# Kernel optimization log

Measured on AMD Instinct MI355X. Metric: run time of the kernel, lower is better.

The kernel has to match this reference:

```python
import jax, jax.numpy as jnp
import numpy as np
import math

L, H, P = 16384, 128, 256


def setup_inputs() -> dict:
    key = jax.random.key(0)
    k = jax.random.split(key, 6)
    return {
        "input_sequence": jax.random.normal(k[0], (L, H), dtype=jnp.float32),
        "A_diag": jax.random.uniform(k[1], (P,), dtype=jnp.float32),
        "B": (jax.random.uniform(k[2], (P, H, 2), dtype=jnp.float32) * 2.0 - 1.0) / math.sqrt(H),
        "C": (jax.random.uniform(k[3], (H, P, 2), dtype=jnp.float32) * 2.0 - 1.0) / math.sqrt(P),
        "D": jax.random.normal(k[4], (H,), dtype=jnp.float32),
        "steps": jax.random.uniform(k[5], (P,), dtype=jnp.float32),
    }


def _binop(qi, qj):
    # 2x2 block-diagonal matrix product + affine state propagation, per channel.
    iA, iB, iC, iD, ib1, ib2 = qi
    jA, jB, jC, jD, jb1, jb2 = qj
    return (
        jA * iA + jB * iC,
        jA * iB + jB * iD,
        jC * iA + jD * iC,
        jC * iB + jD * iD,
        jA * ib1 + jB * ib2 + jb1,
        jC * ib1 + jD * ib2 + jb2,
    )


def reference(input_sequence, A_diag, B, C, D, steps):
    # LinOSS-IM discretization (implicit)
    A = jax.nn.relu(A_diag)                      # (P,)
    dt = jax.nn.sigmoid(steps)                   # (P,)
    Bc = B[..., 0] + 1j * B[..., 1]              # (P,H) complex64
    Cc = C[..., 0] + 1j * C[..., 1]              # (H,P) complex64

    Bu = input_sequence @ Bc.T                   # (L,P) complex64

    schur = 1.0 / (1.0 + dt ** 2 * A)
    M11 = 1.0 - dt ** 2 * A * schur
    M12 = -dt * A * schur
    M21 = dt * schur
    M22 = schur

    ones = jnp.ones((input_sequence.shape[0], A.shape[0]), dtype=input_sequence.dtype)
    F1 = M11 * Bu * dt                           # (L,P) complex
    F2 = M21 * Bu * dt

    elems = (M11 * ones, M12 * ones, M21 * ones, M22 * ones, F1, F2)
    _, _, _, _, _, x2 = jax.lax.associative_scan(_binop, elems)  # scan over L

    ys = jnp.real(x2 @ Cc.T)                     # (L,H)
    return ys + input_sequence * D
```

## Files before the change

### kernel.cpp

```cpp
#include <hip/hip_runtime.h>
#include <math.h>

#define L 16384
#define H 128
#define P 256
#define CL 32
#define NCH (L/CL)
#define GS 16
#define NG (NCH/GS)
#define KDIM 512
#define NBU 512

typedef __attribute__((ext_vector_type(8))) short short8;
typedef __attribute__((ext_vector_type(4))) float f32x4;

__device__ inline unsigned short f2bf(float f){
  union { float f; unsigned u; } v; v.f = f;
  unsigned u = v.u;
  u += 0x7fffu + ((u >> 16) & 1u);
  return (unsigned short)(u >> 16);
}
__device__ inline float bf2f(unsigned short s){
  union { unsigned u; float f; } v; v.u = ((unsigned)s) << 16;
  return v.f;
}

struct Params { float M11,M12,M21,M22,s1,s2; };

__device__ inline Params get_params(const float* A_diag, const float* steps, int p){
  float A = A_diag[p]; A = A > 0.f ? A : 0.f;
  float dt = 1.f/(1.f + expf(-steps[p]));
  float schur = 1.f/(1.f + dt*dt*A);
  Params q;
  q.M11 = 1.f - dt*dt*A*schur;
  q.M12 = -dt*A*schur;
  q.M21 = dt*schur;
  q.M22 = schur;
  q.s1 = q.M11*dt;
  q.s2 = q.M21*dt;
  return q;
}

__device__ inline unsigned long long aload(const unsigned long long* p){
  return __hip_atomic_load((unsigned long long*)p, __ATOMIC_RELAXED,
                           __HIP_MEMORY_SCOPE_AGENT);
}
__device__ inline void apub(unsigned long long* p, unsigned long long v){
  (void)__hip_atomic_exchange(p, v, __ATOMIC_RELAXED, __HIP_MEMORY_SCOPE_AGENT);
}
__device__ inline void fpub(unsigned* p){
  (void)__hip_atomic_exchange(p, 1u, __ATOMIC_RELAXED, __HIP_MEMORY_SCOPE_AGENT);
}
__device__ inline void wait_flag(unsigned* f){
  while (__hip_atomic_load(f, __ATOMIC_RELAXED, __HIP_MEMORY_SCOPE_AGENT) == 0u)
    __builtin_amdgcn_s_sleep(2);
}

__global__ __launch_bounds__(512) void prep_w(const float* __restrict__ B,
                                              const float* __restrict__ Cw,
                                              unsigned short* __restrict__ BWswz,
                                              unsigned short* __restrict__ Bswz,
                                              unsigned* __restrict__ flags){
  int gidx = blockIdx.x*512 + threadIdx.x;
  if (gidx < NCH + NG) flags[gidx] = 0u;
  if (gidx < H*NBU){
    int k = gidx >> 9, n = gidx & 511;
    int p = n & 255, c2 = n >> 8;
    float v = B[((size_t)p*H + k)*2 + c2];
    BWswz[((size_t)(k>>3)*NBU + n)*8 + (k&7)] = f2bf(v);
  } else {
    int g2 = gidx - H*NBU;
    int k = g2 >> 7, n = g2 & 127;
    float v = (k < P) ? Cw[((size_t)n*P + k)*2]
                      : -Cw[((size_t)n*P + (k-P))*2 + 1];
    Bswz[((size_t)(k>>3)*H + n)*8 + (k&7)] = f2bf(v);
  }
}

__global__ __launch_bounds__(512, 4) void linoss_fused(
    const float* __restrict__ in,
    const float* __restrict__ A_diag,
    const float* __restrict__ steps,
    const float* __restrict__ Dv,
    const unsigned short* __restrict__ BWswz,
    const unsigned short* __restrict__ Bswz,
    unsigned long long* __restrict__ finals,
    unsigned long long* __restrict__ gfin,
    unsigned* __restrict__ flag1,
    unsigned* __restrict__ flag2,
    float* __restrict__ out)
{
  __shared__ unsigned short sX[CL][NBU+8];
  const int c   = blockIdx.x;
  const int tid = threadIdx.x;

  {
    int lane = tid & 63, w = tid >> 6;
    int ml = lane & 15, quad = lane >> 4;
    int mt = w & 1, ng = w >> 1;
    int lm0 = mt*16;
    const float* aptr = in + (size_t)(c*CL + lm0 + ml)*H + quad*8;
    short8 av[4];
    #pragma unroll
    for (int ks=0; ks<4; ks++){
      float4 f0 = *(const float4*)(aptr + ks*32);
      float4 f1 = *(const float4*)(aptr + ks*32 + 4);
      union { short8 s; unsigned short u[8]; } o;
      o.u[0]=f2bf(f0.x); o.u[1]=f2bf(f0.y); o.u[2]=f2bf(f0.z); o.u[3]=f2bf(f0.w);
      o.u[4]=f2bf(f1.x); o.u[5]=f2bf(f1.y); o.u[6]=f2bf(f1.z); o.u[7]=f2bf(f1.w);
      av[ks] = o.s;
    }
    f32x4 acc[8];
    #pragma unroll
    for (int t=0;t<8;t++) acc[t] = (f32x4){0.f,0.f,0.f,0.f};
    #pragma unroll
    for (int ks=0; ks<4; ks++){
      #pragma unroll
      for (int t=0;t<8;t++){
        int n0 = (ng*8 + t)*16;
        short8 bv = *(const short8*)(BWswz + ((size_t)(ks*4+quad)*NBU + n0 + ml)*8);
        acc[t] = __builtin_amdgcn_mfma_f32_16x16x32_bf16(av[ks], bv, acc[t], 0, 0, 0);
      }
    }
    #pragma unroll
    for (int t=0;t<8;t++){
      int n = (ng*8+t)*16 + ml;
      #pragma unroll
      for (int r=0;r<4;r++)
        sX[lm0 + quad*4 + r][n] = f2bf(acc[t][r]);
    }
  }
  __syncthreads();

  const int p = tid & 255, part = tid >> 8;
  Params q = get_params(A_diag, steps, p);
  float Ta=q.M11, Tb=q.M12, Tc=q.M21, Td=q.M22;
  #pragma unroll
  for (int s=0;s<5;s++){
    float na=Ta*Ta+Tb*Tc, nb=Ta*Tb+Tb*Td, nc=Tc*Ta+Td*Tc, nd=Tc*Tb+Td*Td;
    Ta=na;Tb=nb;Tc=nc;Td=nd;
  }
  float fx1=0.f, fx2=0.f;
  {
    #pragma unroll
    for (int i=0;i<CL;i++){
      float u = bf2f(sX[i][part*256 + p]);
      float n1 = q.M11*fx1 + q.M12*fx2 + q.s1*u;
      float n2 = q.M21*fx1 + q.M22*fx2 + q.s2*u;
      fx1 = n1; fx2 = n2;
    }
    union { unsigned long long u; float2 f; } w; w.f = make_float2(fx1,fx2);
    apub(&finals[(size_t)(part*NCH + c)*P + p], w.u);
  }
  asm volatile("s_waitcnt vmcnt(0)" ::: "memory");
  __syncthreads();
  if (tid == 0) fpub(&flag1[c]);

  const int g = c >> 4, iw = c & (GS-1);
  const unsigned long long* Fp = finals + (size_t)part*NCH*P + (size_t)g*GS*P + p;

  float z1=0.f, z2v=0.f;
  bool have_z = false;
  if (iw == GS-1){
    if (tid < GS-1) wait_flag(&flag1[g*GS + tid]);
    __syncthreads();
    unsigned long long v[GS-1];
    #pragma unroll
    for (int j=0;j<GS-1;j++) v[j] = aload(Fp + (size_t)j*P);
    #pragma unroll
    for (int j=0;j<GS-1;j++){
      union { unsigned long long u; float2 f; } w; w.u = v[j];
      float n1 = Ta*z1 + Tb*z2v + w.f.x;
      float n2 = Tc*z1 + Td*z2v + w.f.y;
      z1=n1; z2v=n2;
    }
    have_z = true;
    float t1 = Ta*z1 + Tb*z2v + fx1;
    float t2 = Tc*z1 + Td*z2v + fx2;
    union { unsigned long long u; float2 f; } w; w.f = make_float2(t1,t2);
    apub(&gfin[(size_t)(part*NG + g)*P + p], w.u);
    asm volatile("s_waitcnt vmcnt(0)" ::: "memory");
    __syncthreads();
    if (tid == 0) fpub(&flag2[g]);
  }

  float sa=1.f, sb=0.f, sc=0.f, sd=1.f;
  {
    float wa=Ta, wb=Tb, wc=Tc, wd=Td;
    #pragma unroll
    for (int bit=0; bit<4; bit++){
      if ((iw>>bit)&1){
        float na = wa*sa + wb*sc, nb = wa*sb + wb*sd;
        float nc = wc*sa + wd*sc, nd = wc*sb + wd*sd;
        sa=na; sb=nb; sc=nc; sd=nd;
      }
      float qa = wa*wa + wb*wc, qb = wa*wb + wb*wd;
      float qc = wc*wa + wd*wc, qd = wc*wb + wd*wd;
      wa=qa; wb=qb; wc=qc; wd=qd;
    }
  }
  float ga=Ta, gb=Tb, gc=Tc, gd=Td;
  #pragma unroll
  for (int s=0;s<4;s++){
    float na=ga*ga+gb*gc, nb=ga*gb+gb*gd, nc=gc*ga+gd*gc, nd=gc*gb+gd*gd;
    ga=na;gb=nb;gc=nc;gd=nd;
  }

  if (tid < g)                             wait_flag(&flag2[tid]);
  if (!have_z && tid >= 64 && tid < 64+iw) wait_flag(&flag1[g*GS + (tid-64)]);
  __syncthreads();

  {
    float y1=0.f, y2=0.f;
    {
      const unsigned long long* Gp = gfin + (size_t)part*NG*P + p;
      for (int t0=0; t0<g; t0+=8){
        unsigned long long v[8];
        #pragma unroll
        for (int j=0;j<8;j++){
          int jj = t0+j;
          v[j] = (jj < g) ? aload(Gp + (size_t)jj*P) : 0ULL;
        }
        #pragma unroll
        for (int j=0;j<8;j++){
          int jj = t0+j;
          if (jj < g){
            union { unsigned long long u; float2 f; } w; w.u = v[j];
            float n1 = ga*y1 + gb*y2 + w.f.x;
            float n2 = gc*y1 + gd*y2 + w.f.y;
            y1=n1; y2=n2;
          }
        }
      }
    }
    if (!have_z){
      for (int t0=0; t0<iw; t0+=8){
        unsigned long long v[8];
        #pragma unroll
        for (int j=0;j<8;j++){
          int jj = t0+j;
          v[j] = (jj < iw) ? aload(Fp + (size_t)jj*P) : 0ULL;
        }
        #pragma unroll
        for (int j=0;j<8;j++){
          int jj = t0+j;
          if (jj < iw){
            union { unsigned long long u; float2 f; } w; w.u = v[j];
            float n1 = Ta*z1 + Tb*z2v + w.f.x;
            float n2 = Tc*z1 + Td*z2v + w.f.y;
            z1=n1; z2v=n2;
          }
        }
      }
    }
    float x1 = sa*y1 + sb*y2 + z1;
    float x2 = sc*y1 + sd*y2 + z2v;
    #pragma unroll
    for (int i=0;i<CL;i++){
      float u = bf2f(sX[i][part*256 + p]);
      float n1 = q.M11*x1 + q.M12*x2 + q.s1*u;
      float n2 = q.M21*x1 + q.M22*x2 + q.s2*u;
      x1 = n1; x2 = n2;
      sX[i][part*256 + p] = f2bf(x2);
    }
  }
  __syncthreads();

  {
    int lane = tid & 63, w = tid >> 6;
    int ml = lane & 15, quad = lane >> 4;
    int mt = w & 1;
    int ntb = (w >> 1) * 2;
    f32x4 acc[2];
    acc[0] = (f32x4){0.f,0.f,0.f,0.f};
    acc[1] = (f32x4){0.f,0.f,0.f,0.f};
    for (int ks=0; ks<KDIM/32; ks++){
      short8 av = *(const short8*)&sX[mt*16 + ml][ks*32 + quad*8];
      #pragma unroll
      for (int j=0;j<2;j++){
        short8 bv = *(const short8*)(Bswz + ((size_t)(ks*4+quad)*H + (ntb+j)*16 + ml)*8);
        acc[j] = __builtin_amdgcn_mfma_f32_16x16x32_bf16(av, bv, acc[j], 0, 0, 0);
      }
    }
    #pragma unroll
    for (int j=0;j<2;j++){
      int h = (ntb+j)*16 + ml;
      float dv = Dv[h];
      #pragma unroll
      for (int r=0;r<4;r++){
        int l = c*CL + mt*16 + quad*4 + r;
        out[(size_t)l*H + h] = acc[j][r] + in[(size_t)l*H + h]*dv;
      }
    }
  }
}

extern "C" void kernel_launch(void* const* d_in, const int* in_sizes, int n_in,
                              void* d_out, int out_size, void* d_ws, size_t ws_size,
                              hipStream_t stream) {
  const float* in     = (const float*)d_in[0];
  const float* A_diag = (const float*)d_in[1];
  const float* B      = (const float*)d_in[2];
  const float* Cw     = (const float*)d_in[3];
  const float* Dv     = (const float*)d_in[4];
  const float* steps  = (const float*)d_in[5];
  float* out = (float*)d_out;

  unsigned short* BWswz = (unsigned short*)d_ws;
  unsigned short* Bswz  = BWswz + (size_t)H*NBU;
  unsigned long long* finals = (unsigned long long*)(Bswz + (size_t)KDIM*H);
  unsigned long long* gfin   = finals + (size_t)2*NCH*P;
  unsigned* flags = (unsigned*)(gfin + (size_t)2*NG*P);
  unsigned* flag1 = flags;
  unsigned* flag2 = flags + NCH;

  prep_w<<<256, 512, 0, stream>>>(B, Cw, BWswz, Bswz, flags);
  linoss_fused<<<NCH, 512, 0, stream>>>(in, A_diag, steps, Dv, BWswz, Bswz,
                                        finals, gfin, flag1, flag2, out);
}
```

Before: 100.5 us.

## Double chunk length to 64 and fully unroll cross-chunk carry loads

Doubles the per-block chunk length, which halves the number of chunks and groups. That shrinks the inter-block carry chain and the flag synchronization traffic. The warp-to-tile mappings of both MFMA phases are remapped to cover 64 rows, and the power-of-transition exponent is bumped to match. Carry loads from group and chunk finals are now issued all at once into register arrays rather than in batches of 8. The costs are higher register and LDS pressure (occupancy hint lowered from 4 to 2), longer serial in-block scans, and fewer blocks to fill the GPU.

```diff
diff --git a/kernel.cpp b/kernel.cpp
--- a/kernel.cpp
+++ b/kernel.cpp
@@ -4,7 +4,7 @@
 #define L 16384
 #define H 128
 #define P 256
-#define CL 32
+#define CL 64
 #define NCH (L/CL)
 #define GS 16
 #define NG (NCH/GS)
@@ -53,7 +53,7 @@
 }
 __device__ inline void wait_flag(unsigned* f){
   while (__hip_atomic_load(f, __ATOMIC_RELAXED, __HIP_MEMORY_SCOPE_AGENT) == 0u)
-    __builtin_amdgcn_s_sleep(2);
+    __builtin_amdgcn_s_sleep(1);
 }
 
 __global__ __launch_bounds__(512) void prep_w(const float* __restrict__ B,
@@ -77,7 +77,7 @@
   }
 }
 
-__global__ __launch_bounds__(512, 4) void linoss_fused(
+__global__ __launch_bounds__(512, 2) void linoss_fused(
     const float* __restrict__ in,
     const float* __restrict__ A_diag,
     const float* __restrict__ steps,
@@ -97,8 +97,8 @@
   {
     int lane = tid & 63, w = tid >> 6;
     int ml = lane & 15, quad = lane >> 4;
-    int mt = w & 1, ng = w >> 1;
-    int lm0 = mt*16;
+    int rt = w & 3, ch = w >> 2;
+    int lm0 = rt*16;
     const float* aptr = in + (size_t)(c*CL + lm0 + ml)*H + quad*8;
     short8 av[4];
     #pragma unroll
@@ -110,21 +110,21 @@
       o.u[4]=f2bf(f1.x); o.u[5]=f2bf(f1.y); o.u[6]=f2bf(f1.z); o.u[7]=f2bf(f1.w);
       av[ks] = o.s;
     }
-    f32x4 acc[8];
-    #pragma unroll
-    for (int t=0;t<8;t++) acc[t] = (f32x4){0.f,0.f,0.f,0.f};
+    f32x4 acc[16];
+    #pragma unroll
+    for (int t=0;t<16;t++) acc[t] = (f32x4){0.f,0.f,0.f,0.f};
     #pragma unroll
     for (int ks=0; ks<4; ks++){
       #pragma unroll
-      for (int t=0;t<8;t++){
-        int n0 = (ng*8 + t)*16;
+      for (int t=0;t<16;t++){
+        int n0 = ch*256 + t*16;
         short8 bv = *(const short8*)(BWswz + ((size_t)(ks*4+quad)*NBU + n0 + ml)*8);
         acc[t] = __builtin_amdgcn_mfma_f32_16x16x32_bf16(av[ks], bv, acc[t], 0, 0, 0);
       }
     }
     #pragma unroll
-    for (int t=0;t<8;t++){
-      int n = (ng*8+t)*16 + ml;
+    for (int t=0;t<16;t++){
+      int n = ch*256 + t*16 + ml;
       #pragma unroll
       for (int r=0;r<4;r++)
         sX[lm0 + quad*4 + r][n] = f2bf(acc[t][r]);
@@ -136,7 +136,7 @@
   Params q = get_params(A_diag, steps, p);
   float Ta=q.M11, Tb=q.M12, Tc=q.M21, Td=q.M22;
   #pragma unroll
-  for (int s=0;s<5;s++){
+  for (int s=0;s<6;s++){
     float na=Ta*Ta+Tb*Tc, nb=Ta*Tb+Tb*Td, nc=Tc*Ta+Td*Tc, nd=Tc*Tb+Td*Td;
     Ta=na;Tb=nb;Tc=nc;Td=nd;
   }
@@ -211,45 +211,32 @@
   __syncthreads();
 
   {
+    const unsigned long long* Gp = gfin + (size_t)part*NG*P + p;
+    unsigned long long vy[NG-1], vm[GS-1];
+    #pragma unroll
+    for (int j=0;j<NG-1;j++) vy[j] = (j < g) ? aload(Gp + (size_t)j*P) : 0ULL;
+    if (!have_z){
+      #pragma unroll
+      for (int j=0;j<GS-1;j++) vm[j] = (j < iw) ? aload(Fp + (size_t)j*P) : 0ULL;
+    }
     float y1=0.f, y2=0.f;
-    {
-      const unsigned long long* Gp = gfin + (size_t)part*NG*P + p;
-      for (int t0=0; t0<g; t0+=8){
-        unsigned long long v[8];
-        #pragma unroll
-        for (int j=0;j<8;j++){
-          int jj = t0+j;
-          v[j] = (jj < g) ? aload(Gp + (size_t)jj*P) : 0ULL;
-        }
-        #pragma unroll
-        for (int j=0;j<8;j++){
-          int jj = t0+j;
-          if (jj < g){
-            union { unsigned long long u; float2 f; } w; w.u = v[j];
-            float n1 = ga*y1 + gb*y2 + w.f.x;
-            float n2 = gc*y1 + gd*y2 + w.f.y;
-            y1=n1; y2=n2;
-          }
-        }
+    #pragma unroll
+    for (int j=0;j<NG-1;j++){
+      if (j < g){
+        union { unsigned long long u; float2 f; } w; w.u = vy[j];
+        float n1 = ga*y1 + gb*y2 + w.f.x;
+        float n2 = gc*y1 + gd*y2 + w.f.y;
+        y1=n1; y2=n2;
       }
     }
     if (!have_z){
-      for (int t0=0; t0<iw; t0+=8){
-        unsigned long long v[8];
-        #pragma unroll
-        for (int j=0;j<8;j++){
-          int jj = t0+j;
-          v[j] = (jj < iw) ? aload(Fp + (size_t)jj*P) : 0ULL;
-        }
-        #pragma unroll
-        for (int j=0;j<8;j++){
-          int jj = t0+j;
-          if (jj < iw){
-            union { unsigned long long u; float2 f; } w; w.u = v[j];
-            float n1 = Ta*z1 + Tb*z2v + w.f.x;
-            float n2 = Tc*z1 + Td*z2v + w.f.y;
-            z1=n1; z2v=n2;
-          }
+      #pragma unroll
+      for (int j=0;j<GS-1;j++){
+        if (j < iw){
+          union { unsigned long long u; float2 f; } w; w.u = vm[j];
+          float n1 = Ta*z1 + Tb*z2v + w.f.x;
+          float n2 = Tc*z1 + Td*z2v + w.f.y;
+          z1=n1; z2v=n2;
         }
       }
     }
@@ -269,26 +256,26 @@
   {
     int lane = tid & 63, w = tid >> 6;
     int ml = lane & 15, quad = lane >> 4;
-    int mt = w & 1;
-    int ntb = (w >> 1) * 2;
-    f32x4 acc[2];
-    acc[0] = (f32x4){0.f,0.f,0.f,0.f};
-    acc[1] = (f32x4){0.f,0.f,0.f,0.f};
+    int rt2 = w & 3;
+    int nh  = w >> 2;
+    f32x4 acc[4];
+    #pragma unroll
+    for (int j=0;j<4;j++) acc[j] = (f32x4){0.f,0.f,0.f,0.f};
     for (int ks=0; ks<KDIM/32; ks++){
-      short8 av = *(const short8*)&sX[mt*16 + ml][ks*32 + quad*8];
-      #pragma unroll
-      for (int j=0;j<2;j++){
-        short8 bv = *(const short8*)(Bswz + ((size_t)(ks*4+quad)*H + (ntb+j)*16 + ml)*8);
+      short8 av = *(const short8*)&sX[rt2*16 + ml][ks*32 + quad*8];
+      #pragma unroll
+      for (int j=0;j<4;j++){
+        short8 bv = *(const short8*)(Bswz + ((size_t)(ks*4+quad)*H + (nh*4+j)*16 + ml)*8);
         acc[j] = __builtin_amdgcn_mfma_f32_16x16x32_bf16(av, bv, acc[j], 0, 0, 0);
       }
     }
     #pragma unroll
-    for (int j=0;j<2;j++){
-      int h = (ntb+j)*16 + ml;
+    for (int j=0;j<4;j++){
+      int h = (nh*4+j)*16 + ml;
       float dv = Dv[h];
       #pragma unroll
       for (int r=0;r<4;r++){
-        int l = c*CL + mt*16 + quad*4 + r;
+        int l = c*CL + rt2*16 + quad*4 + r;
         out[(size_t)l*H + h] = acc[j][r] + in[(size_t)l*H + h]*dv;
       }
     }
```

Result: faster. 94.36 us (-6.1%).

## Assign chunk IDs by atomic ticket and batch LDS reads in scan loops

Applied to the files above, without the earlier changes.

Each block now takes its chunk index from a global atomic counter instead of blockIdx, so the decoupled look-back cannot wait on chunks whose blocks have not been scheduled yet. The scan loops first read all CL inputs from LDS into registers and write results back in a batch. The group-prefix and in-group loops are fully unrolled with fixed-size loads, and the spin-wait sleep is shortened. This raises register pressure, costs one extra atomic per block, and issues some unneeded loads.

```diff
diff --git a/kernel.cpp b/kernel.cpp
--- a/kernel.cpp
+++ b/kernel.cpp
@@ -53,7 +53,47 @@
 }
 __device__ inline void wait_flag(unsigned* f){
   while (__hip_atomic_load(f, __ATOMIC_RELAXED, __HIP_MEMORY_SCOPE_AGENT) == 0u)
-    __builtin_amdgcn_s_sleep(2);
+    __builtin_amdgcn_s_sleep(1);
+}
+
+__device__ inline void chunk_bu_to_lds(int c, const float* __restrict__ in,
+                                       const unsigned short* __restrict__ BWswz,
+                                       unsigned short (*sBu)[NBU+8]){
+  int tid = threadIdx.x;
+  int lane = tid & 63, w = tid >> 6;
+  int ml = lane & 15, quad = lane >> 4;
+  int mt = w & 1, ng = w >> 1;
+  int lm0 = mt*16;
+  const float* aptr = in + (size_t)(c*CL + lm0 + ml)*H + quad*8;
+  short8 av[4];
+  #pragma unroll
+  for (int ks=0; ks<4; ks++){
+    float4 f0 = *(const float4*)(aptr + ks*32);
+    float4 f1 = *(const float4*)(aptr + ks*32 + 4);
+    union { short8 s; unsigned short u[8]; } o;
+    o.u[0]=f2bf(f0.x); o.u[1]=f2bf(f0.y); o.u[2]=f2bf(f0.z); o.u[3]=f2bf(f0.w);
+    o.u[4]=f2bf(f1.x); o.u[5]=f2bf(f1.y); o.u[6]=f2bf(f1.z); o.u[7]=f2bf(f1.w);
+    av[ks] = o.s;
+  }
+  f32x4 acc[8];
+  #pragma unroll
+  for (int t=0;t<8;t++) acc[t] = (f32x4){0.f,0.f,0.f,0.f};
+  #pragma unroll
+  for (int ks=0; ks<4; ks++){
+    #pragma unroll
+    for (int t=0;t<8;t++){
+      int n0 = (ng*8 + t)*16;
+      short8 bv = *(const short8*)(BWswz + ((size_t)(ks*4+quad)*NBU + n0 + ml)*8);
+      acc[t] = __builtin_amdgcn_mfma_f32_16x16x32_bf16(av[ks], bv, acc[t], 0, 0, 0);
+    }
+  }
+  #pragma unroll
+  for (int t=0;t<8;t++){
+    int n = (ng*8+t)*16 + ml;
+    #pragma unroll
+    for (int r=0;r<4;r++)
+      sBu[lm0 + quad*4 + r][n] = f2bf(acc[t][r]);
+  }
 }
 
 __global__ __launch_bounds__(512) void prep_w(const float* __restrict__ B,
@@ -62,7 +102,7 @@
                                               unsigned short* __restrict__ Bswz,
                                               unsigned* __restrict__ flags){
   int gidx = blockIdx.x*512 + threadIdx.x;
-  if (gidx < NCH + NG) flags[gidx] = 0u;
+  if (gidx < NCH + NG + 1) flags[gidx] = 0u;
   if (gidx < H*NBU){
     int k = gidx >> 9, n = gidx & 511;
     int p = n & 255, c2 = n >> 8;
@@ -88,48 +128,19 @@
     unsigned long long* __restrict__ gfin,
     unsigned* __restrict__ flag1,
     unsigned* __restrict__ flag2,
+    unsigned* __restrict__ counter,
     float* __restrict__ out)
 {
   __shared__ unsigned short sX[CL][NBU+8];
-  const int c   = blockIdx.x;
+  __shared__ int s_cid;
   const int tid = threadIdx.x;
-
-  {
-    int lane = tid & 63, w = tid >> 6;
-    int ml = lane & 15, quad = lane >> 4;
-    int mt = w & 1, ng = w >> 1;
-    int lm0 = mt*16;
-    const float* aptr = in + (size_t)(c*CL + lm0 + ml)*H + quad*8;
-    short8 av[4];
-    #pragma unroll
-    for (int ks=0; ks<4; ks++){
-      float4 f0 = *(const float4*)(aptr + ks*32);
-      float4 f1 = *(const float4*)(aptr + ks*32 + 4);
-      union { short8 s; unsigned short u[8]; } o;
-      o.u[0]=f2bf(f0.x); o.u[1]=f2bf(f0.y); o.u[2]=f2bf(f0.z); o.u[3]=f2bf(f0.w);
-      o.u[4]=f2bf(f1.x); o.u[5]=f2bf(f1.y); o.u[6]=f2bf(f1.z); o.u[7]=f2bf(f1.w);
-      av[ks] = o.s;
-    }
-    f32x4 acc[8];
-    #pragma unroll
-    for (int t=0;t<8;t++) acc[t] = (f32x4){0.f,0.f,0.f,0.f};
-    #pragma unroll
-    for (int ks=0; ks<4; ks++){
-      #pragma unroll
-      for (int t=0;t<8;t++){
-        int n0 = (ng*8 + t)*16;
-        short8 bv = *(const short8*)(BWswz + ((size_t)(ks*4+quad)*NBU + n0 + ml)*8);
-        acc[t] = __builtin_amdgcn_mfma_f32_16x16x32_bf16(av[ks], bv, acc[t], 0, 0, 0);
-      }
-    }
-    #pragma unroll
-    for (int t=0;t<8;t++){
-      int n = (ng*8+t)*16 + ml;
-      #pragma unroll
-      for (int r=0;r<4;r++)
-        sX[lm0 + quad*4 + r][n] = f2bf(acc[t][r]);
-    }
-  }
+  if (tid == 0)
+    s_cid = (int)__hip_atomic_fetch_add(counter, 1u, __ATOMIC_RELAXED,
+                                        __HIP_MEMORY_SCOPE_AGENT);
+  __syncthreads();
+  const int c = s_cid;
+
+  chunk_bu_to_lds(c, in, BWswz, sX);
   __syncthreads();
 
   const int p = tid & 255, part = tid >> 8;
@@ -142,13 +153,17 @@
   }
   float fx1=0.f, fx2=0.f;
   {
+    float u[CL];
+    #pragma unroll
+    for (int i=0;i<CL;i++) u[i] = bf2f(sX[i][part*256 + p]);
     #pragma unroll
     for (int i=0;i<CL;i++){
-      float u = bf2f(sX[i][part*256 + p]);
-      float n1 = q.M11*fx1 + q.M12*fx2 + q.s1*u;
-      float n2 = q.M21*fx1 + q.M22*fx2 + q.s2*u;
+      float n1 = q.M11*fx1 + q.M12*fx2 + q.s1*u[i];
+      float n2 = q.M21*fx1 + q.M22*fx2 + q.s2*u[i];
       fx1 = n1; fx2 = n2;
     }
+  }
+  {
     union { unsigned long long u; float2 f; } w; w.f = make_float2(fx1,fx2);
     apub(&finals[(size_t)(part*NCH + c)*P + p], w.u);
   }
@@ -214,16 +229,14 @@
     float y1=0.f, y2=0.f;
     {
       const unsigned long long* Gp = gfin + (size_t)part*NG*P + p;
-      for (int t0=0; t0<g; t0+=8){
-        unsigned long long v[8];
+      #pragma unroll
+      for (int half=0; half<2; half++){
+        unsigned long long v[16];
         #pragma unroll
-        for (int j=0;j<8;j++){
-          int jj = t0+j;
-          v[j] = (jj < g) ? aload(Gp + (size_t)jj*P) : 0ULL;
-        }
+        for (int j=0;j<16;j++) v[j] = aload(Gp + (size_t)(half*16+j)*P);
         #pragma unroll
-        for (int j=0;j<8;j++){
-          int jj = t0+j;
+        for (int j=0;j<16;j++){
+          int jj = half*16+j;
           if (jj < g){
             union { unsigned long long u; float2 f; } w; w.u = v[j];
             float n1 = ga*y1 + gb*y2 + w.f.x;
@@ -234,35 +247,34 @@
       }
     }
     if (!have_z){
-      for (int t0=0; t0<iw; t0+=8){
-        unsigned long long v[8];
-        #pragma unroll
-        for (int j=0;j<8;j++){
-          int jj = t0+j;
-          v[j] = (jj < iw) ? aload(Fp + (size_t)jj*P) : 0ULL;
-        }
-        #pragma unroll
-        for (int j=0;j<8;j++){
-          int jj = t0+j;
-          if (jj < iw){
-            union { unsigned long long u; float2 f; } w; w.u = v[j];
-            float n1 = Ta*z1 + Tb*z2v + w.f.x;
-            float n2 = Tc*z1 + Td*z2v + w.f.y;
-            z1=n1; z2v=n2;
-          }
+      unsigned long long v[GS-1];
+      #pragma unroll
+      for (int j=0;j<GS-1;j++) v[j] = aload(Fp + (size_t)j*P);
+      #pragma unroll
+      for (int j=0;j<GS-1;j++){
+        if (j < iw){
+          union { unsigned long long u; float2 f; } w; w.u = v[j];
+          float n1 = Ta*z1 + Tb*z2v + w.f.x;
+          float n2 = Tc*z1 + Td*z2v + w.f.y;
+          z1=n1; z2v=n2;
         }
       }
     }
     float x1 = sa*y1 + sb*y2 + z1;
     float x2 = sc*y1 + sd*y2 + z2v;
+    float u[CL];
+    #pragma unroll
+    for (int i=0;i<CL;i++) u[i] = bf2f(sX[i][part*256 + p]);
+    unsigned short hw[CL];
     #pragma unroll
     for (int i=0;i<CL;i++){
-      float u = bf2f(sX[i][part*256 + p]);
-      float n1 = q.M11*x1 + q.M12*x2 + q.s1*u;
-      float n2 = q.M21*x1 + q.M22*x2 + q.s2*u;
+      float n1 = q.M11*x1 + q.M12*x2 + q.s1*u[i];
+      float n2 = q.M21*x1 + q.M22*x2 + q.s2*u[i];
       x1 = n1; x2 = n2;
-      sX[i][part*256 + p] = f2bf(x2);
-    }
+      hw[i] = f2bf(x2);
+    }
+    #pragma unroll
+    for (int i=0;i<CL;i++) sX[i][part*256 + p] = hw[i];
   }
   __syncthreads();
 
@@ -313,8 +325,9 @@
   unsigned* flags = (unsigned*)(gfin + (size_t)2*NG*P);
   unsigned* flag1 = flags;
   unsigned* flag2 = flags + NCH;
+  unsigned* counter = flags + NCH + NG;
 
   prep_w<<<256, 512, 0, stream>>>(B, Cw, BWswz, Bswz, flags);
   linoss_fused<<<NCH, 512, 0, stream>>>(in, A_diag, steps, Dv, BWswz, Bswz,
-                                        finals, gfin, flag1, flag2, out);
-}
+                                        finals, gfin, flag1, flag2, counter, out);
+}
```

New measurement: 105.2 us. +4.7%, slower.
